# Kernel tuning notes

Measured on AMD Instinct MI355X. Metric: run time of the kernel, lower is better.

The kernel has to match this reference:

```python
import jax, jax.numpy as jnp
import numpy as np


def Qmat(V):
    """Chain of Householder reflections: Q = I @ H(v_0) @ ... @ H(v_{d-1}).

    Faithful to the source: columns of V are normalized, H(v) = I - 2 v v^T.
    M @ H(v) == M - 2 (M v) v^T, so each step is a matvec + rank-1 update
    (same math as the source's full GEMM, O(d^2) per step instead of O(d^3)).
    """
    d = V.shape[0]
    # torch.norm(V.T, 2, dim=1) == L2 norm of each column of V
    norms = jnp.linalg.norm(V, axis=0)  # (d,)
    Vn = V / norms[None, :]

    def step(M, v):
        Mv = M @ v                        # (d,)
        return M - 2.0 * jnp.outer(Mv, v), None

    M0 = jnp.eye(d, dtype=V.dtype)
    M, _ = jax.lax.scan(step, M0, Vn.T)   # iterate over columns v_i
    return M


def setup_inputs() -> dict:
    key = jax.random.key(0)
    k1, k2 = jax.random.split(key)
    ci, co = 1024, 2048
    U = 0.05 * jax.random.normal(k1, (ci, ci), dtype=jnp.float32)
    V = 0.05 * jax.random.normal(k2, (co, co), dtype=jnp.float32)
    return {"U": U, "V": V}


def reference(U, V):
    ci, co = U.shape[0], V.shape[0]
    Qu = Qmat(U)  # (ci, ci) orthogonal
    Qv = Qmat(V)  # (co, co) orthogonal
    if ci < co:
        weight = Qu @ Qv[:ci, :]      # (ci, co)
    else:
        weight = Qu[:, :co] @ Qv      # (ci, co)
    return weight
```

## Files before the change

kernel.cpp:

```cpp
#include <hip/hip_runtime.h>
#include <hip/hip_bf16.h>
#include <cstdint>

#define CI 1024
#define CO 2048
#define NB 256

typedef float  fx4  __attribute__((ext_vector_type(4)));
typedef short  s16x4 __attribute__((ext_vector_type(4)));
typedef short  s16x8 __attribute__((ext_vector_type(8)));
typedef unsigned short u16;

#define MFMA(a,b,c) __builtin_amdgcn_mfma_f32_16x16x32_bf16((a),(b),(c),0,0,0)

__device__ __forceinline__ u16 f2b(float x) {
    __hip_bfloat16 h = __float2bfloat16(x);
    return __builtin_bit_cast(u16, h);
}
__device__ __forceinline__ float b2f(u16 u) {
    __hip_bfloat16 h = __builtin_bit_cast(__hip_bfloat16, u);
    return __bfloat162float(h);
}


__global__ __launch_bounds__(256) void colnorm2(const float* __restrict__ M, float* __restrict__ n2, int d) {
    int c = blockIdx.x * 256 + threadIdx.x;
    int r0 = blockIdx.y * 64;
    float s = 0.0f;
    for (int r = r0; r < r0 + 64; ++r) {
        float v = M[(size_t)r * d + c];
        s = fmaf(v, v, s);
    }
    atomicAdd(&n2[c], s);
}

__global__ __launch_bounds__(256) void init_W(float* __restrict__ W) {
    int c = blockIdx.x * 256 + threadIdx.x;
    int r = blockIdx.y;
    W[(size_t)r * CO + c] = (c == r) ? 1.0f : 0.0f;
}

__global__ __launch_bounds__(256) void reduce_S(const float* __restrict__ src, float* __restrict__ dst, int split) {
    int b = blockIdx.y;
    int i = blockIdx.x * 256 + threadIdx.x;
    const float* p = src + (size_t)b * split * NB * NB + i;
    float acc = 0.0f;
    for (int s = 0; s < split; ++s) acc += p[(size_t)s * NB * NB];
    dst[(size_t)b * NB * NB + i] = acc;
}

__global__ __launch_bounds__(256) void trans_planes(const float* __restrict__ X, int d,
                                                    u16* __restrict__ Th, u16* __restrict__ Tl) {
    size_t zo = (size_t)blockIdx.z * d * d;
    const float* Xz = X + zo;
    u16* Thz = Th + zo;
    u16* Tlz = Tl + zo;
    __shared__ float tile[32][33];
    int t = threadIdx.x;
    int r = t >> 3, c4 = (t & 7) * 4;
    int bx = blockIdx.x, by = blockIdx.y;
    fx4 v = *(const fx4*)(Xz + (size_t)(by * 32 + r) * d + bx * 32 + c4);
    tile[r][c4 + 0] = v[0]; tile[r][c4 + 1] = v[1]; tile[r][c4 + 2] = v[2]; tile[r][c4 + 3] = v[3];
    __syncthreads();
    int a = bx * 32 + r;
    u16 h[4], l[4];
    #pragma unroll
    for (int j = 0; j < 4; ++j) {
        float f = tile[c4 + j][r];
        u16 hb = f2b(f);
        h[j] = hb;
        l[j] = f2b(f - b2f(hb));
    }
    size_t o = (size_t)a * d + by * 32 + c4;
    *(s16x4*)&Thz[o] = *(s16x4*)&h[0];
    *(s16x4*)&Tlz[o] = *(s16x4*)&l[0];
}

__global__ __launch_bounds__(64) void trinv_scaled(const float* __restrict__ Sall, float* __restrict__ Mtall,
                                                   const float* __restrict__ n2u, const float* __restrict__ n2v) {
    int j = blockIdx.x;
    int b = blockIdx.y;
    const float* S = Sall + (size_t)b * NB * NB;
    float* Mt = Mtall + (size_t)b * NB * NB;
    const float* n2 = (b < 4) ? (n2u + b * NB) : (n2v + (size_t)(b - 4) * NB);
    int l = threadIdx.x;
    float in0 = 1.0f / sqrtf(n2[l]);
    float in1 = 1.0f / sqrtf(n2[l + 64]);
    float in2 = 1.0f / sqrtf(n2[l + 128]);
    float in3 = 1.0f / sqrtf(n2[l + 192]);
    float invnj = 1.0f / sqrtf(n2[j]);
    float i20 = in0 * in0, i21 = in1 * in1, i22 = in2 * in2, i23 = in3 * in3;
    float x0 = 0, x1 = 0, x2 = 0, x3 = 0;
    float a0 = 0, a1 = 0, a2 = 0, a3 = 0;
    int jq = j >> 6, jr = j & 63;
    if (l == jr) {
        float yj = 2.0f * invnj;
        if (jq == 0) x0 = yj; else if (jq == 1) x1 = yj; else if (jq == 2) x2 = yj; else x3 = yj;
    }
    int jpad = (j + 7) & ~7;
    float q00=0,q01=0,q02=0,q03=0, q10=0,q11=0,q12=0,q13=0;
    float q20=0,q21=0,q22=0,q23=0, q30=0,q31=0,q32=0,q33=0;
    float q40=0,q41=0,q42=0,q43=0, q50=0,q51=0,q52=0,q53=0;
    float q60=0,q61=0,q62=0,q63=0, q70=0,q71=0,q72=0,q73=0;
#define LOADROW(Q0,Q1,Q2,Q3, ROW) \
    { int _r = (ROW); if (_r >= 1 && _r <= j) { const float* Sp = S + (size_t)_r * NB; \
        Q0 = Sp[l]; Q1 = Sp[l+64]; Q2 = Sp[l+128]; Q3 = Sp[l+192]; } }
    LOADROW(q00,q01,q02,q03, jpad - 0)
    LOADROW(q10,q11,q12,q13, jpad - 1)
    LOADROW(q20,q21,q22,q23, jpad - 2)
    LOADROW(q30,q31,q32,q33, jpad - 3)
    LOADROW(q40,q41,q42,q43, jpad - 4)
    LOADROW(q50,q51,q52,q53, jpad - 5)
    LOADROW(q60,q61,q62,q63, jpad - 6)
    LOADROW(q70,q71,q72,q73, jpad - 7)
#define STEP(Q0,Q1,Q2,Q3) { \
    int kq = k >> 6, kr = k & 63; \
    float yk; \
    if      (kq == 0) yk = __shfl(x0, kr); \
    else if (kq == 1) yk = __shfl(x1, kr); \
    else if (kq == 2) yk = __shfl(x2, kr); \
    else              yk = __shfl(x3, kr); \
    a0 = fmaf(Q0, yk, a0); a1 = fmaf(Q1, yk, a1); \
    a2 = fmaf(Q2, yk, a2); a3 = fmaf(Q3, yk, a3); \
    int i = k - 1; int iq = i >> 6, ir = i & 63; \
    if (k <= j && l == ir) { \
        if      (iq == 0) x0 = -2.0f * i20 * a0; \
        else if (iq == 1) x1 = -2.0f * i21 * a1; \
        else if (iq == 2) x2 = -2.0f * i22 * a2; \
        else              x3 = -2.0f * i23 * a3; \
    } \
    int pr = k - 8; \
    if (pr >= 1) { const float* Sp = S + (size_t)pr * NB; \
        Q0 = Sp[l]; Q1 = Sp[l+64]; Q2 = Sp[l+128]; Q3 = Sp[l+192]; } \
    --k; }
    int k = jpad;
    int ngroups = jpad >> 3;
    for (int g = 0; g < ngroups; ++g) {
        STEP(q00,q01,q02,q03)
        STEP(q10,q11,q12,q13)
        STEP(q20,q21,q22,q23)
        STEP(q30,q31,q32,q33)
        STEP(q40,q41,q42,q43)
        STEP(q50,q51,q52,q53)
        STEP(q60,q61,q62,q63)
        STEP(q70,q71,q72,q73)
    }
#undef STEP
#undef LOADROW
    float* Mr = Mt + (size_t)j * NB;
    Mr[l      ] = x0 * invnj;
    Mr[l +  64] = x1 * invnj;
    Mr[l + 128] = x2 * invnj;
    Mr[l + 192] = x3 * invnj;
}


__device__ __forceinline__ void mma_step(const u16 Ah[][40], const u16 Al[][40],
                                         const u16 Bh[][40], const u16 Bl[][40],
                                         int wr, int wc, int lane, fx4 acc[2][2]) {
    int kb = (lane >> 4) * 8;
    int rl = lane & 15;
    s16x8 ah[2], al[2], bh[2], bl[2];
    #pragma unroll
    for (int f = 0; f < 2; ++f) {
        int ra = wr * 32 + f * 16 + rl;
        s16x4 p = *(const s16x4*)&Ah[ra][kb];
        s16x4 q = *(const s16x4*)&Ah[ra][kb + 4];
        ah[f] = __builtin_shufflevector(p, q, 0,1,2,3,4,5,6,7);
        p = *(const s16x4*)&Al[ra][kb];
        q = *(const s16x4*)&Al[ra][kb + 4];
        al[f] = __builtin_shufflevector(p, q, 0,1,2,3,4,5,6,7);
        int rb = wc * 32 + f * 16 + rl;
        p = *(const s16x4*)&Bh[rb][kb];
        q = *(const s16x4*)&Bh[rb][kb + 4];
        bh[f] = __builtin_shufflevector(p, q, 0,1,2,3,4,5,6,7);
        p = *(const s16x4*)&Bl[rb][kb];
        q = *(const s16x4*)&Bl[rb][kb + 4];
        bl[f] = __builtin_shufflevector(p, q, 0,1,2,3,4,5,6,7);
    }
    #pragma unroll
    for (int i = 0; i < 2; ++i)
        #pragma unroll
        for (int j = 0; j < 2; ++j) {
            acc[i][j] = MFMA(ah[i], bh[j], acc[i][j]);
            acc[i][j] = MFMA(ah[i], bl[j], acc[i][j]);
            acc[i][j] = MFMA(al[i], bh[j], acc[i][j]);
        }
}

template<int NPART>
__device__ __forceinline__ void stage_f32(const float* __restrict__ A, int ldA, size_t pstride,
                                          int m0, int k0, int t, u16 Dh[][40], u16 Dl[][40]) {
    int row = t >> 2, kc = (t & 3) * 8;
    const float* p = A + (size_t)(m0 + row) * ldA + k0 + kc;
    fx4 v0 = *(const fx4*)p;
    fx4 v1 = *(const fx4*)(p + 4);
    #pragma unroll
    for (int s = 1; s < NPART; ++s) {
        const float* q = p + (size_t)s * pstride;
        v0 += *(const fx4*)q;
        v1 += *(const fx4*)(q + 4);
    }
    u16 h[8], l[8];
    #pragma unroll
    for (int j = 0; j < 8; ++j) {
        float f = (j < 4) ? v0[j] : v1[j - 4];
        u16 hb = f2b(f);
        h[j] = hb;
        l[j] = f2b(f - b2f(hb));
    }
    *(s16x4*)&Dh[row][kc]     = *(s16x4*)&h[0];
    *(s16x4*)&Dh[row][kc + 4] = *(s16x4*)&h[4];
    *(s16x4*)&Dl[row][kc]     = *(s16x4*)&l[0];
    *(s16x4*)&Dl[row][kc + 4] = *(s16x4*)&l[4];
}

__device__ __forceinline__ void stage_planes(const u16* __restrict__ Ph, const u16* __restrict__ Pl, int ld,
                                             int n0, int k0, int t, u16 Dh[][40], u16 Dl[][40]) {
    int row = t >> 2, kc = (t & 3) * 8;
    size_t o = (size_t)(n0 + row) * ld + k0 + kc;
    s16x4 h0 = *(const s16x4*)(Ph + o);
    s16x4 h1 = *(const s16x4*)(Ph + o + 4);
    s16x4 l0 = *(const s16x4*)(Pl + o);
    s16x4 l1 = *(const s16x4*)(Pl + o + 4);
    *(s16x4*)&Dh[row][kc]     = h0;
    *(s16x4*)&Dh[row][kc + 4] = h1;
    *(s16x4*)&Dl[row][kc]     = l0;
    *(s16x4*)&Dl[row][kc + 4] = l1;
}

__global__ __launch_bounds__(256) void gram_mfma(const u16* __restrict__ Xh, const u16* __restrict__ Xl,
                                                 int d, int split, int chunk, float* __restrict__ Sp) {
    int z = blockIdx.z;
    int zb = z / split, ks = z % split;
    int c0 = zb * NB, kb = ks * chunk;
    float* S = Sp + (size_t)z * NB * NB;
    __shared__ u16 Ah[64][40], Al[64][40], Bh[64][40], Bl[64][40];
    int t = threadIdx.x, lane = t & 63, w = t >> 6, wr = w >> 1, wc = w & 1;
    int i0 = blockIdx.y * 64, j0 = blockIdx.x * 64;
    fx4 acc[2][2] = {};
    for (int k0 = kb; k0 < kb + chunk; k0 += 32) {
        stage_planes(Xh, Xl, d, c0 + i0, k0, t, Ah, Al);
        stage_planes(Xh, Xl, d, c0 + j0, k0, t, Bh, Bl);
        __syncthreads();
        mma_step(Ah, Al, Bh, Bl, wr, wc, lane, acc);
        __syncthreads();
    }
    #pragma unroll
    for (int fr = 0; fr < 2; ++fr)
        #pragma unroll
        for (int fc = 0; fc < 2; ++fc) {
            int row = i0 + wr * 32 + fr * 16 + ((lane >> 4) << 2);
            int col = j0 + wc * 32 + fc * 16 + (lane & 15);
            #pragma unroll
            for (int r = 0; r < 4; ++r)
                S[(size_t)(row + r) * NB + col] = acc[fr][fc][r];
        }
}

__global__ __launch_bounds__(256) void tbt_mfma(const float* __restrict__ RAW, int d,
                                                const u16* __restrict__ Mh, const u16* __restrict__ Ml,
                                                u16* __restrict__ TBh, u16* __restrict__ TBl) {
    int z = blockIdx.z;
    int c0 = z * NB;
    const u16* Mhz = Mh + (size_t)z * NB * NB;
    const u16* Mlz = Ml + (size_t)z * NB * NB;
    u16* Th = TBh + (size_t)z * d * NB;
    u16* Tl = TBl + (size_t)z * d * NB;
    __shared__ u16 Ah[64][40], Al[64][40], Bh[64][40], Bl[64][40];
    int t = threadIdx.x, lane = t & 63, w = t >> 6, wr = w >> 1, wc = w & 1;
    int m0 = blockIdx.y * 64, n0 = blockIdx.x * 64;
    fx4 acc[2][2] = {};
    for (int k0 = 0; k0 < NB; k0 += 32) {
        stage_f32<1>(RAW + c0, d, 0, m0, k0, t, Ah, Al);
        stage_planes(Mhz, Mlz, NB, n0, k0, t, Bh, Bl);
        __syncthreads();
        mma_step(Ah, Al, Bh, Bl, wr, wc, lane, acc);
        __syncthreads();
    }
    #pragma unroll
    for (int fr = 0; fr < 2; ++fr)
        #pragma unroll
        for (int fc = 0; fc < 2; ++fc) {
            int row = m0 + wr * 32 + fr * 16 + ((lane >> 4) << 2);
            int col = n0 + wc * 32 + fc * 16 + (lane & 15);
            #pragma unroll
            for (int r = 0; r < 4; ++r) {
                float f = acc[fr][fc][r];
                u16 hb = f2b(f);
                Th[(size_t)(row + r) * NB + col] = hb;
                Tl[(size_t)(row + r) * NB + col] = f2b(f - b2f(hb));
            }
        }
}

__global__ __launch_bounds__(256) void chain_part_mfma(const float* __restrict__ W,
                                                       const u16* __restrict__ Bth, const u16* __restrict__ Btl,
                                                       int ldB, float* __restrict__ Cparts, int kchunk) {
    int z = blockIdx.z;
    float* C = Cparts + (size_t)z * CI * NB;
    int kb = z * kchunk;
    __shared__ u16 Ah[64][40], Al[64][40], Bh[64][40], Bl[64][40];
    int t = threadIdx.x, lane = t & 63, w = t >> 6, wr = w >> 1, wc = w & 1;
    int m0 = blockIdx.y * 64, n0 = blockIdx.x * 64;
    fx4 acc[2][2] = {};
    for (int k0 = kb; k0 < kb + kchunk; k0 += 32) {
        stage_f32<1>(W, CO, 0, m0, k0, t, Ah, Al);
        stage_planes(Bth, Btl, ldB, n0, k0, t, Bh, Bl);
        __syncthreads();
        mma_step(Ah, Al, Bh, Bl, wr, wc, lane, acc);
        __syncthreads();
    }
    #pragma unroll
    for (int fr = 0; fr < 2; ++fr)
        #pragma unroll
        for (int fc = 0; fc < 2; ++fc) {
            int row = m0 + wr * 32 + fr * 16 + ((lane >> 4) << 2);
            int col = n0 + wc * 32 + fc * 16 + (lane & 15);
            #pragma unroll
            for (int r = 0; r < 4; ++r)
                C[(size_t)(row + r) * NB + col] = acc[fr][fc][r];
        }
}

template<int NPART>
__global__ __launch_bounds__(256) void chain_sub_mfma(const float* __restrict__ A, int ldA, size_t pstride,
                                                      const u16* __restrict__ TBh, const u16* __restrict__ TBl,
                                                      float* __restrict__ W) {
    __shared__ u16 Ah[64][40], Al[64][40], Bh[64][40], Bl[64][40];
    int t = threadIdx.x, lane = t & 63, w = t >> 6, wr = w >> 1, wc = w & 1;
    int m0 = blockIdx.y * 64, n0 = blockIdx.x * 64;
    fx4 acc[2][2] = {};
    for (int k0 = 0; k0 < NB; k0 += 32) {
        stage_f32<NPART>(A, ldA, pstride, m0, k0, t, Ah, Al);
        stage_planes(TBh, TBl, NB, n0, k0, t, Bh, Bl);
        __syncthreads();
        mma_step(Ah, Al, Bh, Bl, wr, wc, lane, acc);
        __syncthreads();
    }
    #pragma unroll
    for (int fr = 0; fr < 2; ++fr)
        #pragma unroll
        for (int fc = 0; fc < 2; ++fc) {
            int row = m0 + wr * 32 + fr * 16 + ((lane >> 4) << 2);
            int col = n0 + wc * 32 + fc * 16 + (lane & 15);
            #pragma unroll
            for (int r = 0; r < 4; ++r) {
                float* p = W + (size_t)(row + r) * CO + col;
                *p -= acc[fr][fc][r];
            }
        }
}

extern "C" void kernel_launch(void* const* d_in, const int* in_sizes, int n_in,
                              void* d_out, int out_size, void* d_ws, size_t ws_size,
                              hipStream_t stream) {
    const float* U = (const float*)d_in[0];
    const float* V = (const float*)d_in[1];
    float* W = (float*)d_out;

    char* ws = (char*)d_ws;
    float* P0p  = (float*)(ws);
    float* S    = (float*)(ws + ((size_t)8  << 20));
    float* Mt   = (float*)(ws + ((size_t)11 << 20));
    u16*   Mh   = (u16*)  (ws + ((size_t)14 << 20));
    u16*   Ml   = (u16*)  (ws + ((size_t)16 << 20));
    u16*   TBh  = (u16*)  (ws + ((size_t)18 << 20));
    u16*   TBl  = (u16*)  (ws + ((size_t)28 << 20));
    u16*   Uth  = (u16*)  (ws + ((size_t)38 << 20));
    u16*   Utl  = (u16*)  (ws + ((size_t)40 << 20));
    u16*   Vth  = (u16*)  (ws + ((size_t)42 << 20));
    u16*   Vtl  = (u16*)  (ws + ((size_t)50 << 20));
    float* n2u  = (float*)(ws + ((size_t)58 << 20));
    float* n2v  = n2u + CI;
    float* SpU  = (float*)(ws + ((size_t)18 << 20));
    float* SpV  = (float*)(ws + ((size_t)22 << 20));

    float* Su = S;  float* Sv = S + (size_t)4 * NB * NB;
    u16* TBhU = TBh;                       u16* TBlU = TBl;
    u16* TBhV = TBh + (size_t)4 * CI * NB; u16* TBlV = TBl + (size_t)4 * CI * NB;

    hipMemsetAsync(n2u, 0, (CI + CO) * sizeof(float), stream);
    colnorm2<<<dim3(CI / 256, CI / 64), dim3(256), 0, stream>>>(U, n2u, CI);
    colnorm2<<<dim3(CO / 256, CO / 64), dim3(256), 0, stream>>>(V, n2v, CO);

    trans_planes<<<dim3(CI / 32, CI / 32, 1), dim3(256), 0, stream>>>(U, CI, Uth, Utl);
    trans_planes<<<dim3(CO / 32, CO / 32, 1), dim3(256), 0, stream>>>(V, CO, Vth, Vtl);

    gram_mfma<<<dim3(4, 4, 4 * 4), dim3(256), 0, stream>>>(Uth, Utl, CI, 4, CI / 4, SpU);
    gram_mfma<<<dim3(4, 4, 8 * 8), dim3(256), 0, stream>>>(Vth, Vtl, CO, 8, CO / 8, SpV);
    reduce_S<<<dim3(NB * NB / 256, 4), dim3(256), 0, stream>>>(SpU, Su, 4);
    reduce_S<<<dim3(NB * NB / 256, 8), dim3(256), 0, stream>>>(SpV, Sv, 8);
    trinv_scaled<<<dim3(NB, 12), dim3(64), 0, stream>>>(S, Mt, n2u, n2v);

    trans_planes<<<dim3(NB / 32, NB / 32, 12), dim3(256), 0, stream>>>(Mt, NB, Mh, Ml);

    tbt_mfma<<<dim3(4, CI / 64, 4), dim3(256), 0, stream>>>(U, CI, Mh, Ml, TBhU, TBlU);
    tbt_mfma<<<dim3(4, CO / 64, 8), dim3(256), 0, stream>>>(V, CO, Mh + (size_t)4 * NB * NB,
                                                            Ml + (size_t)4 * NB * NB, TBhV, TBlV);

    init_W<<<dim3(CO / 256, CI), dim3(256), 0, stream>>>(W);

    chain_sub_mfma<1><<<dim3(CI / 64, CI / 64), dim3(256), 0, stream>>>(
        U, CI, 0, TBhU, TBlU, W);
    for (int ib = 1; ib < CI / NB; ++ib) {
        chain_part_mfma<<<dim3(4, CI / 64, 4), dim3(256), 0, stream>>>(
            W, Uth + (size_t)ib * NB * CI, Utl + (size_t)ib * NB * CI, CI, P0p, CI / 4);
        chain_sub_mfma<4><<<dim3(CI / 64, CI / 64), dim3(256), 0, stream>>>(
            P0p, NB, (size_t)CI * NB, TBhU + (size_t)ib * CI * NB, TBlU + (size_t)ib * CI * NB, W);
    }
    for (int ib = 0; ib < CO / NB; ++ib) {
        chain_part_mfma<<<dim3(4, CI / 64, 8), dim3(256), 0, stream>>>(
            W, Vth + (size_t)ib * NB * CO, Vtl + (size_t)ib * NB * CO, CO, P0p, CO / 8);
        chain_sub_mfma<8><<<dim3(CO / 64, CI / 64), dim3(256), 0, stream>>>(
            P0p, NB, (size_t)CI * NB, TBhV + (size_t)ib * CO * NB, TBlV + (size_t)ib * CO * NB, W);
    }
}
```

Baseline: 467.4 us.

## Blocked triangular inverse via 64-wide diagonal solves and GEMM merges; pre-reduce chain partials

Replaces the serial 256-step per-column triangular solve with independent 64x64 diagonal block inversions followed by GEMM-based block merges (64→128→256). The aim is to cut the long sequential dependency chain in the compact-WY T computation. It also reduces the chain partial sums once into bf16 hi/lo planes before the subtract GEMM, so each sub-GEMM block no longer re-reads and re-sums every fp32 partial. The cost is extra launches, a memset and a temp buffer, plus a different order of float accumulation.

```diff
diff --git a/kernel.cpp b/kernel.cpp
--- a/kernel.cpp
+++ b/kernel.cpp
@@ -76,84 +76,120 @@
     *(s16x4*)&Tlz[o] = *(s16x4*)&l[0];
 }
 
-__global__ __launch_bounds__(64) void trinv_scaled(const float* __restrict__ Sall, float* __restrict__ Mtall,
-                                                   const float* __restrict__ n2u, const float* __restrict__ n2v) {
-    int j = blockIdx.x;
+__global__ __launch_bounds__(256) void scale_S(float* __restrict__ S,
+                                               const float* __restrict__ n2u, const float* __restrict__ n2v) {
+    int j = blockIdx.x, b = blockIdx.y, i = threadIdx.x;
+    const float* n2 = (b < 4) ? (n2u + b * NB) : (n2v + (size_t)(b - 4) * NB);
+    float inv = (1.0f / sqrtf(n2[j])) * (1.0f / sqrtf(n2[i]));
+    S[(size_t)b * NB * NB + (size_t)j * NB + i] *= inv;
+}
+
+__global__ __launch_bounds__(64) void diag_inv64(const float* __restrict__ Ssc, float* __restrict__ Tt) {
+    int cg = blockIdx.x;
     int b = blockIdx.y;
-    const float* S = Sall + (size_t)b * NB * NB;
-    float* Mt = Mtall + (size_t)b * NB * NB;
-    const float* n2 = (b < 4) ? (n2u + b * NB) : (n2v + (size_t)(b - 4) * NB);
+    int d = cg >> 6, j = cg & 63;
+    const float* S = Ssc + (size_t)b * NB * NB + (size_t)(d * 64) * NB + d * 64;
+    float* Trow = Tt + (size_t)b * NB * NB + (size_t)(d * 64 + j) * NB + d * 64;
     int l = threadIdx.x;
-    float in0 = 1.0f / sqrtf(n2[l]);
-    float in1 = 1.0f / sqrtf(n2[l + 64]);
-    float in2 = 1.0f / sqrtf(n2[l + 128]);
-    float in3 = 1.0f / sqrtf(n2[l + 192]);
-    float invnj = 1.0f / sqrtf(n2[j]);
-    float i20 = in0 * in0, i21 = in1 * in1, i22 = in2 * in2, i23 = in3 * in3;
-    float x0 = 0, x1 = 0, x2 = 0, x3 = 0;
-    float a0 = 0, a1 = 0, a2 = 0, a3 = 0;
-    int jq = j >> 6, jr = j & 63;
-    if (l == jr) {
-        float yj = 2.0f * invnj;
-        if (jq == 0) x0 = yj; else if (jq == 1) x1 = yj; else if (jq == 2) x2 = yj; else x3 = yj;
-    }
+    float x = (l == j) ? 2.0f : 0.0f;
+    float a = 0.0f;
     int jpad = (j + 7) & ~7;
-    float q00=0,q01=0,q02=0,q03=0, q10=0,q11=0,q12=0,q13=0;
-    float q20=0,q21=0,q22=0,q23=0, q30=0,q31=0,q32=0,q33=0;
-    float q40=0,q41=0,q42=0,q43=0, q50=0,q51=0,q52=0,q53=0;
-    float q60=0,q61=0,q62=0,q63=0, q70=0,q71=0,q72=0,q73=0;
-#define LOADROW(Q0,Q1,Q2,Q3, ROW) \
-    { int _r = (ROW); if (_r >= 1 && _r <= j) { const float* Sp = S + (size_t)_r * NB; \
-        Q0 = Sp[l]; Q1 = Sp[l+64]; Q2 = Sp[l+128]; Q3 = Sp[l+192]; } }
-    LOADROW(q00,q01,q02,q03, jpad - 0)
-    LOADROW(q10,q11,q12,q13, jpad - 1)
-    LOADROW(q20,q21,q22,q23, jpad - 2)
-    LOADROW(q30,q31,q32,q33, jpad - 3)
-    LOADROW(q40,q41,q42,q43, jpad - 4)
-    LOADROW(q50,q51,q52,q53, jpad - 5)
-    LOADROW(q60,q61,q62,q63, jpad - 6)
-    LOADROW(q70,q71,q72,q73, jpad - 7)
-#define STEP(Q0,Q1,Q2,Q3) { \
-    int kq = k >> 6, kr = k & 63; \
-    float yk; \
-    if      (kq == 0) yk = __shfl(x0, kr); \
-    else if (kq == 1) yk = __shfl(x1, kr); \
-    else if (kq == 2) yk = __shfl(x2, kr); \
-    else              yk = __shfl(x3, kr); \
-    a0 = fmaf(Q0, yk, a0); a1 = fmaf(Q1, yk, a1); \
-    a2 = fmaf(Q2, yk, a2); a3 = fmaf(Q3, yk, a3); \
-    int i = k - 1; int iq = i >> 6, ir = i & 63; \
-    if (k <= j && l == ir) { \
-        if      (iq == 0) x0 = -2.0f * i20 * a0; \
-        else if (iq == 1) x1 = -2.0f * i21 * a1; \
-        else if (iq == 2) x2 = -2.0f * i22 * a2; \
-        else              x3 = -2.0f * i23 * a3; \
-    } \
+    float q0=0,q1=0,q2=0,q3=0,q4=0,q5=0,q6=0,q7=0;
+#define LR(Q, R) { int _r = (R); if (_r >= 1 && _r <= j) Q = S[(size_t)_r * NB + l]; }
+    LR(q0, jpad - 0) LR(q1, jpad - 1) LR(q2, jpad - 2) LR(q3, jpad - 3)
+    LR(q4, jpad - 4) LR(q5, jpad - 5) LR(q6, jpad - 6) LR(q7, jpad - 7)
+#define ST(Q) { \
+    float yk = __shfl(x, k); \
+    a = fmaf(Q, yk, a); \
+    if (k <= j && l == k - 1) x = -2.0f * a; \
     int pr = k - 8; \
-    if (pr >= 1) { const float* Sp = S + (size_t)pr * NB; \
-        Q0 = Sp[l]; Q1 = Sp[l+64]; Q2 = Sp[l+128]; Q3 = Sp[l+192]; } \
+    if (pr >= 1) Q = S[(size_t)pr * NB + l]; \
     --k; }
     int k = jpad;
-    int ngroups = jpad >> 3;
-    for (int g = 0; g < ngroups; ++g) {
-        STEP(q00,q01,q02,q03)
-        STEP(q10,q11,q12,q13)
-        STEP(q20,q21,q22,q23)
-        STEP(q30,q31,q32,q33)
-        STEP(q40,q41,q42,q43)
-        STEP(q50,q51,q52,q53)
-        STEP(q60,q61,q62,q63)
-        STEP(q70,q71,q72,q73)
-    }
-#undef STEP
-#undef LOADROW
-    float* Mr = Mt + (size_t)j * NB;
-    Mr[l      ] = x0 * invnj;
-    Mr[l +  64] = x1 * invnj;
-    Mr[l + 128] = x2 * invnj;
-    Mr[l + 192] = x3 * invnj;
-}
-
+    int ng = jpad >> 3;
+    for (int g = 0; g < ng; ++g) {
+        ST(q0) ST(q1) ST(q2) ST(q3) ST(q4) ST(q5) ST(q6) ST(q7)
+    }
+#undef ST
+#undef LR
+    Trow[l] = x;
+}
+
+__global__ __launch_bounds__(128) void merge_gemm(const float* __restrict__ Ssc, float* __restrict__ Tt,
+                                                  float* __restrict__ tmp, int mode) {
+    int z = blockIdx.z;
+    const float* A; const float* B; float* C;
+    int lda, ldb, ldc, K; float sgn;
+    if (mode == 0) {
+        int b = z >> 1, p = z & 1; int c0 = p * 128, r0 = c0 + 64;
+        A = Ssc + (size_t)b * NB * NB + (size_t)r0 * NB + c0; lda = NB;
+        B = Tt  + (size_t)b * NB * NB + (size_t)c0 * NB + c0; ldb = NB;
+        C = tmp + (size_t)z * 4096; ldc = 64; K = 64; sgn = 1.0f;
+    } else if (mode == 1) {
+        int b = z >> 1, p = z & 1; int c0 = p * 128, r0 = c0 + 64;
+        A = Tt  + (size_t)b * NB * NB + (size_t)r0 * NB + r0; lda = NB;
+        B = tmp + (size_t)z * 4096; ldb = 64;
+        C = Tt  + (size_t)b * NB * NB + (size_t)r0 * NB + c0; ldc = NB; K = 64; sgn = -1.0f;
+    } else if (mode == 2) {
+        A = Ssc + (size_t)z * NB * NB + (size_t)128 * NB; lda = NB;
+        B = Tt  + (size_t)z * NB * NB; ldb = NB;
+        C = tmp + (size_t)z * 16384; ldc = 128; K = 128; sgn = 1.0f;
+    } else {
+        A = Tt  + (size_t)z * NB * NB + (size_t)128 * NB + 128; lda = NB;
+        B = tmp + (size_t)z * 16384; ldb = 128;
+        C = Tt  + (size_t)z * NB * NB + (size_t)128 * NB; ldc = NB; K = 128; sgn = -1.0f;
+    }
+    int m0 = blockIdx.y * 64, n0 = blockIdx.x * 64;
+    __shared__ float As[16][64];
+    __shared__ float Bs[16][64];
+    int tid = threadIdx.x;
+    int tm = (tid >> 4) * 8, tn = (tid & 15) * 4;
+    int ar = tid >> 2, ac = (tid & 3) * 4;
+    int bk = tid >> 4, bn = (tid & 15) * 4;
+    float acc[8][4] = {};
+    for (int k0 = 0; k0 < K; k0 += 16) {
+        #pragma unroll
+        for (int p = 0; p < 2; ++p) {
+            int r = ar + p * 32;
+            fx4 av = *(const fx4*)(A + (size_t)(m0 + r) * lda + k0 + ac);
+            As[ac + 0][r] = av[0]; As[ac + 1][r] = av[1]; As[ac + 2][r] = av[2]; As[ac + 3][r] = av[3];
+        }
+        #pragma unroll
+        for (int p = 0; p < 2; ++p) {
+            int kk = bk + p * 8;
+            *(fx4*)&Bs[kk][bn] = *(const fx4*)(B + (size_t)(k0 + kk) * ldb + n0 + bn);
+        }
+        __syncthreads();
+        #pragma unroll
+        for (int k = 0; k < 16; ++k) {
+            fx4 alo = *(const fx4*)&As[k][tm];
+            fx4 ahi = *(const fx4*)&As[k][tm + 4];
+            fx4 bv  = *(const fx4*)&Bs[k][tn];
+            float a[8] = {alo[0], alo[1], alo[2], alo[3], ahi[0], ahi[1], ahi[2], ahi[3]};
+            float bb[4] = {bv[0], bv[1], bv[2], bv[3]};
+            #pragma unroll
+            for (int i = 0; i < 8; ++i)
+                #pragma unroll
+                for (int jj = 0; jj < 4; ++jj) acc[i][jj] = fmaf(a[i], bb[jj], acc[i][jj]);
+        }
+        __syncthreads();
+    }
+    #pragma unroll
+    for (int i = 0; i < 8; ++i) {
+        fx4 v = { sgn * acc[i][0], sgn * acc[i][1], sgn * acc[i][2], sgn * acc[i][3] };
+        *(fx4*)(C + (size_t)(m0 + tm + i) * ldc + n0 + tn) = v;
+    }
+}
+
+__global__ __launch_bounds__(256) void mt_scale(const float* __restrict__ Tt, float* __restrict__ Mt,
+                                                const float* __restrict__ n2u, const float* __restrict__ n2v) {
+    int j = blockIdx.x, b = blockIdx.y, i = threadIdx.x;
+    const float* n2 = (b < 4) ? (n2u + b * NB) : (n2v + (size_t)(b - 4) * NB);
+    float v = 0.0f;
+    if (i <= j)
+        v = Tt[(size_t)b * NB * NB + (size_t)j * NB + i] * (1.0f / sqrtf(n2[i])) * (1.0f / sqrtf(n2[j]));
+    Mt[(size_t)b * NB * NB + (size_t)j * NB + i] = v;
+}
 
 __device__ __forceinline__ void mma_step(const u16 Ah[][40], const u16 Al[][40],
                                          const u16 Bh[][40], const u16 Bl[][40],
@@ -323,6 +359,58 @@
         }
 }
 
+__global__ __launch_bounds__(256) void reduce_planes(const float* __restrict__ src, int npart,
+                                                     u16* __restrict__ Ph, u16* __restrict__ Pl) {
+    size_t idx = ((size_t)blockIdx.x * 256 + threadIdx.x) * 8;
+    fx4 v0 = *(const fx4*)(src + idx);
+    fx4 v1 = *(const fx4*)(src + idx + 4);
+    for (int s = 1; s < npart; ++s) {
+        const float* p = src + (size_t)s * CI * NB + idx;
+        v0 += *(const fx4*)p;
+        v1 += *(const fx4*)(p + 4);
+    }
+    u16 h[8], l[8];
+    #pragma unroll
+    for (int j = 0; j < 8; ++j) {
+        float f = (j < 4) ? v0[j] : v1[j - 4];
+        u16 hb = f2b(f);
+        h[j] = hb;
+        l[j] = f2b(f - b2f(hb));
+    }
+    *(s16x4*)&Ph[idx]     = *(s16x4*)&h[0];
+    *(s16x4*)&Ph[idx + 4] = *(s16x4*)&h[4];
+    *(s16x4*)&Pl[idx]     = *(s16x4*)&l[0];
+    *(s16x4*)&Pl[idx + 4] = *(s16x4*)&l[4];
+}
+
+__global__ __launch_bounds__(256) void chain_sub_pl(const u16* __restrict__ Ph, const u16* __restrict__ Pl,
+                                                    const u16* __restrict__ TBh, const u16* __restrict__ TBl,
+                                                    float* __restrict__ W) {
+    __shared__ u16 Ah[64][40], Al[64][40], Bh[64][40], Bl[64][40];
+    int t = threadIdx.x, lane = t & 63, w = t >> 6, wr = w >> 1, wc = w & 1;
+    int m0 = blockIdx.y * 64, n0 = blockIdx.x * 64;
+    fx4 acc[2][2] = {};
+    for (int k0 = 0; k0 < NB; k0 += 32) {
+        stage_planes(Ph, Pl, NB, m0, k0, t, Ah, Al);
+        stage_planes(TBh, TBl, NB, n0, k0, t, Bh, Bl);
+        __syncthreads();
+        mma_step(Ah, Al, Bh, Bl, wr, wc, lane, acc);
+        __syncthreads();
+    }
+    #pragma unroll
+    for (int fr = 0; fr < 2; ++fr)
+        #pragma unroll
+        for (int fc = 0; fc < 2; ++fc) {
+            int row = m0 + wr * 32 + fr * 16 + ((lane >> 4) << 2);
+            int col = n0 + wc * 32 + fc * 16 + (lane & 15);
+            #pragma unroll
+            for (int r = 0; r < 4; ++r) {
+                float* p = W + (size_t)(row + r) * CO + col;
+                *p -= acc[fr][fc][r];
+            }
+        }
+}
+
 template<int NPART>
 __global__ __launch_bounds__(256) void chain_sub_mfma(const float* __restrict__ A, int ldA, size_t pstride,
                                                       const u16* __restrict__ TBh, const u16* __restrict__ TBl,
@@ -361,10 +449,13 @@
 
     char* ws = (char*)d_ws;
     float* P0p  = (float*)(ws);
+    float* tmp  = (float*)(ws);
     float* S    = (float*)(ws + ((size_t)8  << 20));
-    float* Mt   = (float*)(ws + ((size_t)11 << 20));
-    u16*   Mh   = (u16*)  (ws + ((size_t)14 << 20));
-    u16*   Ml   = (u16*)  (ws + ((size_t)16 << 20));
+    float* Tt   = (float*)(ws + ((size_t)11 << 20));
+    u16*   Mh   = (u16*)  (ws + ((size_t)14336 << 10));
+    u16*   Ml   = (u16*)  (ws + ((size_t)15872 << 10));
+    u16*   Ph   = (u16*)  (ws + ((size_t)17408 << 10));
+    u16*   Pl   = (u16*)  (ws + ((size_t)17920 << 10));
     u16*   TBh  = (u16*)  (ws + ((size_t)18 << 20));
     u16*   TBl  = (u16*)  (ws + ((size_t)28 << 20));
     u16*   Uth  = (u16*)  (ws + ((size_t)38 << 20));
@@ -377,6 +468,7 @@
     float* SpV  = (float*)(ws + ((size_t)22 << 20));
 
     float* Su = S;  float* Sv = S + (size_t)4 * NB * NB;
+    float* Mt = S;
     u16* TBhU = TBh;                       u16* TBlU = TBl;
     u16* TBhV = TBh + (size_t)4 * CI * NB; u16* TBlV = TBl + (size_t)4 * CI * NB;
 
@@ -391,28 +483,36 @@
     gram_mfma<<<dim3(4, 4, 8 * 8), dim3(256), 0, stream>>>(Vth, Vtl, CO, 8, CO / 8, SpV);
     reduce_S<<<dim3(NB * NB / 256, 4), dim3(256), 0, stream>>>(SpU, Su, 4);
     reduce_S<<<dim3(NB * NB / 256, 8), dim3(256), 0, stream>>>(SpV, Sv, 8);
-    trinv_scaled<<<dim3(NB, 12), dim3(64), 0, stream>>>(S, Mt, n2u, n2v);
+
+    scale_S<<<dim3(NB, 12), dim3(256), 0, stream>>>(S, n2u, n2v);
+    hipMemsetAsync(Tt, 0, (size_t)12 * NB * NB * sizeof(float), stream);
+    diag_inv64<<<dim3(NB, 12), dim3(64), 0, stream>>>(S, Tt);
+    merge_gemm<<<dim3(1, 1, 24), dim3(128), 0, stream>>>(S, Tt, tmp, 0);
+    merge_gemm<<<dim3(1, 1, 24), dim3(128), 0, stream>>>(S, Tt, tmp, 1);
+    merge_gemm<<<dim3(2, 2, 12), dim3(128), 0, stream>>>(S, Tt, tmp, 2);
+    merge_gemm<<<dim3(2, 2, 12), dim3(128), 0, stream>>>(S, Tt, tmp, 3);
+    mt_scale<<<dim3(NB, 12), dim3(256), 0, stream>>>(Tt, Mt, n2u, n2v);
 
     trans_planes<<<dim3(NB / 32, NB / 32, 12), dim3(256), 0, stream>>>(Mt, NB, Mh, Ml);
-
     tbt_mfma<<<dim3(4, CI / 64, 4), dim3(256), 0, stream>>>(U, CI, Mh, Ml, TBhU, TBlU);
     tbt_mfma<<<dim3(4, CO / 64, 8), dim3(256), 0, stream>>>(V, CO, Mh + (size_t)4 * NB * NB,
                                                             Ml + (size_t)4 * NB * NB, TBhV, TBlV);
 
     init_W<<<dim3(CO / 256, CI), dim3(256), 0, stream>>>(W);
 
-    chain_sub_mfma<1><<<dim3(CI / 64, CI / 64), dim3(256), 0, stream>>>(
-        U, CI, 0, TBhU, TBlU, W);
+    chain_sub_mfma<1><<<dim3(CI / 64, CI / 64), dim3(256), 0, stream>>>(U, CI, 0, TBhU, TBlU, W);
     for (int ib = 1; ib < CI / NB; ++ib) {
         chain_part_mfma<<<dim3(4, CI / 64, 4), dim3(256), 0, stream>>>(
             W, Uth + (size_t)ib * NB * CI, Utl + (size_t)ib * NB * CI, CI, P0p, CI / 4);
-        chain_sub_mfma<4><<<dim3(CI / 64, CI / 64), dim3(256), 0, stream>>>(
-            P0p, NB, (size_t)CI * NB, TBhU + (size_t)ib * CI * NB, TBlU + (size_t)ib * CI * NB, W);
+        reduce_planes<<<dim3(CI * NB / 2048), dim3(256), 0, stream>>>(P0p, 4, Ph, Pl);
+        chain_sub_pl<<<dim3(CI / 64, CI / 64), dim3(256), 0, stream>>>(
+            Ph, Pl, TBhU + (size_t)ib * CI * NB, TBlU + (size_t)ib * CI * NB, W);
     }
     for (int ib = 0; ib < CO / NB; ++ib) {
         chain_part_mfma<<<dim3(4, CI / 64, 8), dim3(256), 0, stream>>>(
             W, Vth + (size_t)ib * NB * CO, Vtl + (size_t)ib * NB * CO, CO, P0p, CO / 8);
-        chain_sub_mfma<8><<<dim3(CO / 64, CI / 64), dim3(256), 0, stream>>>(
-            P0p, NB, (size_t)CI * NB, TBhV + (size_t)ib * CO * NB, TBlV + (size_t)ib * CO * NB, W);
-    }
-}
+        reduce_planes<<<dim3(CI * NB / 2048), dim3(256), 0, stream>>>(P0p, 8, Ph, Pl);
+        chain_sub_pl<<<dim3(CO / 64, CI / 64), dim3(256), 0, stream>>>(
+            Ph, Pl, TBhV + (size_t)ib * CO * NB, TBlV + (size_t)ib * CO * NB, W);
+    }
+}
```

New measurement: 414.4 us. -11.3%, faster.
